# Kernel tuning notes

Measured on AMD Instinct MI355X. Metric: run time of the kernel, lower is better.

Reference implementation:

```python
import jax, jax.numpy as jnp
from jax import lax
import numpy as np

# GConv2d config (matches init_kwargs)
OUT_TRANSFORMS = 4  # rotations: 0, 90, 180, 270 degrees
STRIDE = 1
PADDING = 1


def setup_inputs() -> dict:
    key = jax.random.key(0)
    k1, k2, k3, k4 = jax.random.split(key, 4)
    B, IC_EFF, H, W = 16, 256, 64, 64   # IC_EFF = in_channels * in_transformations
    OC, K, F = 64, 4, 3                 # out_channels, num_dynamic_kernels, filter_size
    x = jax.random.normal(k1, (B, IC_EFF, H, W), dtype=jnp.float32)
    W_fc = jax.random.normal(k2, (K, IC_EFF), dtype=jnp.float32) * (1.0 / np.sqrt(IC_EFF))
    b_fc = jnp.zeros((K,), dtype=jnp.float32)
    kernel_bank = jax.random.normal(k3, (K, OC, IC_EFF, F, F), dtype=jnp.float32)
    return {"x": x, "W_fc": W_fc, "b_fc": b_fc, "kernel_bank": kernel_bank}


def reference(x, W_fc, b_fc, kernel_bank):
    B, C, H, W = x.shape
    # Dynamic routing: global average pool -> linear -> softmax over kernel bank
    pooled = x.mean(axis=(2, 3))                      # [B, C]
    coeffs = jax.nn.softmax(pooled @ W_fc.T + b_fc, axis=1)  # [B, K]
    # Sample-specific base kernels: mix of kernel bank
    base = jnp.einsum('bk,kocij->bocij', coeffs, kernel_bank)  # [B, oc, C, f, f]
    # P4 orientation expansion: rotate kernel spatially, stack along out-channels
    oriented = jnp.concatenate(
        [jnp.rot90(base, k, axes=(-2, -1)) for k in range(OUT_TRANSFORMS)], axis=1
    )  # [B, 4*oc, C, f, f]
    O, f = oriented.shape[1], oriented.shape[-1]
    # Batched per-sample conv via grouped convolution (one launch instead of B)
    xg = x.reshape(1, B * C, H, W)
    kg = oriented.reshape(B * O, C, f, f)
    out = lax.conv_general_dilated(
        xg, kg,
        window_strides=(STRIDE, STRIDE),
        padding=[(PADDING, PADDING), (PADDING, PADDING)],
        dimension_numbers=('NCHW', 'OIHW', 'NCHW'),
        feature_group_count=B,
    )  # [1, B*O, H', W']
    Ho, Wo = out.shape[-2], out.shape[-1]
    return out.reshape(B, O, Ho, Wo)
```

## Files before the change

### kernel.cpp

```cpp
#include <hip/hip_runtime.h>

#define B_  16
#define C_  256
#define O_  256

typedef short    bf16x8 __attribute__((ext_vector_type(8)));
typedef float    f32x16 __attribute__((ext_vector_type(16)));
typedef unsigned u32x4  __attribute__((ext_vector_type(4)));
typedef unsigned u32x2  __attribute__((ext_vector_type(2)));

#define XROW_SH  1056
#define XBC_SH   (66 * XROW_SH)
#define XT_BYTES ((size_t)B_ * 16 * XBC_SH * 2)

#define WTILE_SH 9216
#define WORP_BYTES ((size_t)B_ * 16 * 4 * WTILE_SH * 2)

#define XBUF_SH  10752

__device__ __forceinline__ unsigned cvtpk(float lo, float hi) {
    unsigned r;
    asm("v_cvt_pk_bf16_f32 %0, %1, %2" : "=v"(r) : "v"(lo), "v"(hi));
    return r;
}

__device__ __forceinline__ void gload16(const void* g, void* l) {
    __builtin_amdgcn_global_load_lds(
        (const __attribute__((address_space(1))) unsigned int*)g,
        (__attribute__((address_space(3))) unsigned int*)l, 16, 0, 0);
}

__global__ __launch_bounds__(256) void xprep_kernel(const float* __restrict__ x,
                                                    short* __restrict__ xT,
                                                    float* __restrict__ pooled4) {
    const int cg = blockIdx.x;
    const int b  = blockIdx.y;
    const int z  = blockIdx.z;
    const int t  = threadIdx.x;
    const int lane = t & 63, wv = t >> 6;
    const int cc = cg >> 1, lh = cg & 1;

    short* xTb = xT + (size_t)(b * 16 + cc) * XBC_SH;
    const float* xb = x + ((size_t)(b * C_ + cg * 8) << 12);

    {
        u32x4 zv = {0, 0, 0, 0};
        if (t < 32) {
            int r   = z * 16 + 1 + (t >> 1);
            int col = (t & 1) ? 65 : 0;
            *(u32x4*)&xTb[r * XROW_SH + lh * 528 + col * 8] = zv;
        }
        if (z == 0 || z == 3) {
            int row = (z == 0) ? 0 : 65;
            if (t < 66) *(u32x4*)&xTb[row * XROW_SH + lh * 528 + t * 8] = zv;
        }
    }

    float s[8] = {0.f, 0.f, 0.f, 0.f, 0.f, 0.f, 0.f, 0.f};
    const int px = lane;
#pragma unroll
    for (int r = 0; r < 4; ++r) {
        const int row = z * 16 + wv * 4 + r;
        const float* src = xb + row * 64 + px;
        float v[8];
#pragma unroll
        for (int i = 0; i < 8; ++i) { v[i] = src[(size_t)i << 12]; s[i] += v[i]; }
        u32x4 d = { cvtpk(v[0], v[1]), cvtpk(v[2], v[3]),
                    cvtpk(v[4], v[5]), cvtpk(v[6], v[7]) };
        *(u32x4*)&xTb[(row + 1) * XROW_SH + lh * 528 + (px + 1) * 8] = d;
    }

#pragma unroll
    for (int i = 0; i < 8; ++i)
#pragma unroll
        for (int off = 32; off; off >>= 1) s[i] += __shfl_xor(s[i], off, 64);

    __shared__ float pr[4][8];
    if (lane == 0) {
#pragma unroll
        for (int i = 0; i < 8; ++i) pr[wv][i] = s[i];
    }
    __syncthreads();
    if (t < 8) {
        float v = pr[0][t] + pr[1][t] + pr[2][t] + pr[3][t];
        pooled4[(z * B_ + b) * C_ + cg * 8 + t] = v * (1.0f / 4096.0f);
    }
}

__global__ __launch_bounds__(256) void mix_kernel(const float* __restrict__ bank,
                                                  const float* __restrict__ pooled4,
                                                  const float* __restrict__ W_fc,
                                                  const float* __restrict__ b_fc,
                                                  short* __restrict__ worp) {
    const int b  = blockIdx.x;
    const int cc = blockIdx.y;
    const int t  = threadIdx.x, lane = t & 63, wid = t >> 6;

    __shared__ float bankL[4 * 64 * 37];
    __shared__ float lg[4];

    {
        float s = 0.f;
#pragma unroll
        for (int q = 0; q < 4; ++q) {
            int c = lane * 4 + q;
            float pv = pooled4[b * C_ + c] + pooled4[(B_ + b) * C_ + c]
                     + pooled4[(2 * B_ + b) * C_ + c] + pooled4[(3 * B_ + b) * C_ + c];
            s += pv * W_fc[wid * C_ + c];
        }
#pragma unroll
        for (int off = 32; off; off >>= 1) s += __shfl_down(s, off, 64);
        if (lane == 0) lg[wid] = s + b_fc[wid];
    }
    __syncthreads();
    float l0 = lg[0], l1 = lg[1], l2 = lg[2], l3 = lg[3];
    float mx = fmaxf(fmaxf(l0, l1), fmaxf(l2, l3));
    float e0 = expf(l0 - mx), e1 = expf(l1 - mx), e2 = expf(l2 - mx), e3 = expf(l3 - mx);
    float inv = 1.f / (e0 + e1 + e2 + e3);
    const float cf0 = e0 * inv, cf1 = e1 * inv, cf2 = e2 * inv, cf3 = e3 * inv;

    const int oq  = t >> 6;
    const int o64 = t & 63;

    for (int sub = 0; sub < 4; ++sub) {
        __syncthreads();
        for (int i = t; i < 9216; i += 256) {
            int run = i / 36, e = i % 36;
            bankL[run * 37 + e] = bank[((size_t)run * C_ + cc * 16 + sub * 4) * 9 + e];
        }
        __syncthreads();

        const int lhs = sub >> 1;
        const float* bp = &bankL[o64 * 37];
#pragma unroll
        for (int ti = 0; ti < 3; ++ti)
#pragma unroll
            for (int tj = 0; tj < 3; ++tj) {
                int si, sj;
                if      (oq == 0) { si = ti;     sj = tj;     }
                else if (oq == 1) { si = tj;     sj = 2 - ti; }
                else if (oq == 2) { si = 2 - ti; sj = 2 - tj; }
                else              { si = 2 - tj; sj = ti;     }
                const int sij = si * 3 + sj;
                float v[4];
#pragma unroll
                for (int c4 = 0; c4 < 4; ++c4) {
                    const float* q = bp + c4 * 9 + sij;
                    v[c4] = cf0 * q[0] + cf1 * q[64 * 37] + cf2 * q[2 * 64 * 37]
                          + cf3 * q[3 * 64 * 37];
                }
                u32x2 d = { cvtpk(v[0], v[1]), cvtpk(v[2], v[3]) };
                size_t base = (((((size_t)(b * 16 + cc) * 4 + oq) * 9 + (ti * 3 + tj)) * 2
                                + lhs) * 64 + o64) * 8 + (sub & 1) * 4;
                *(u32x2*)&worp[base] = d;
            }
    }
}

__global__ __launch_bounds__(256, 2)
void conv_mfma(const short* __restrict__ xT, const short* __restrict__ worp,
               float* __restrict__ out) {
    __shared__ short lds[2 * XBUF_SH];

    const int g    = blockIdx.x;
    const int w    = (g & 7) * 64 + (g >> 3);
    const int oq   = w & 3;
    const int m    = w >> 2;
    const int rowt = m & 7;
    const int b    = m >> 3;
    const int y0   = rowt * 8;

    const int t    = threadIdx.x;
    const int lane = t & 63;
    const int wid  = t >> 6;
    const int l31  = lane & 31;
    const int lh   = lane >> 5;

    const char* xsrcB = (const char*)xT
        + ((size_t)(b * 16) * XBC_SH + (size_t)y0 * XROW_SH) * 2 + lane * 16;
    const short* wq = worp + (((size_t)(b * 16) * 4) + oq) * WTILE_SH;

#define STAGE(ccc, p)                                                           \
    { const char* xs = xsrcB + (size_t)(ccc) * (XBC_SH * 2);                    \
      char* xd = (char*)lds + (p) * (XBUF_SH * 2);                              \
      for (int u = wid; u < 21; u += 4) gload16(xs + u * 1024, xd + u * 1024); }

#define BRD(r, s) (*(const bf16x8*)&xcur[(((r) * 2 + lh) * 66 + (s) + l31) * 8])

    f32x16 acc0[4] = {}, acc1[4] = {};

    STAGE(0, 0);
    __syncthreads();

    for (int cc = 0; cc < 16; ++cc) {
        const int p = cc & 1;
        const short* wsc = wq + (size_t)cc * (4 * WTILE_SH);

        bf16x8 Af[3][3][2];
#pragma unroll
        for (int i = 0; i < 3; ++i)
#pragma unroll
            for (int j = 0; j < 3; ++j)
#pragma unroll
                for (int oh = 0; oh < 2; ++oh)
                    Af[i][j][oh] = *(const bf16x8*)
                        (wsc + (((i * 3 + j) * 2 + lh) * 64 + oh * 32 + l31) * 8);

        if (cc < 15) STAGE(cc + 1, p ^ 1);

        const short* xcur = lds + p * XBUF_SH;
        __builtin_amdgcn_s_setprio(1);
#pragma unroll
        for (int i = 0; i < 3; ++i)
#pragma unroll
            for (int j = 0; j < 3; ++j) {
                bf16x8 B00 = BRD(2 * wid + i,     j);
                bf16x8 B01 = BRD(2 * wid + i,     32 + j);
                bf16x8 B10 = BRD(2 * wid + i + 1, j);
                bf16x8 B11 = BRD(2 * wid + i + 1, 32 + j);
                acc0[0] = __builtin_amdgcn_mfma_f32_32x32x16_bf16(Af[i][j][0], B00, acc0[0], 0, 0, 0);
                acc1[0] = __builtin_amdgcn_mfma_f32_32x32x16_bf16(Af[i][j][1], B00, acc1[0], 0, 0, 0);
                acc0[1] = __builtin_amdgcn_mfma_f32_32x32x16_bf16(Af[i][j][0], B01, acc0[1], 0, 0, 0);
                acc1[1] = __builtin_amdgcn_mfma_f32_32x32x16_bf16(Af[i][j][1], B01, acc1[1], 0, 0, 0);
                acc0[2] = __builtin_amdgcn_mfma_f32_32x32x16_bf16(Af[i][j][0], B10, acc0[2], 0, 0, 0);
                acc1[2] = __builtin_amdgcn_mfma_f32_32x32x16_bf16(Af[i][j][1], B10, acc1[2], 0, 0, 0);
                acc0[3] = __builtin_amdgcn_mfma_f32_32x32x16_bf16(Af[i][j][0], B11, acc0[3], 0, 0, 0);
                acc1[3] = __builtin_amdgcn_mfma_f32_32x32x16_bf16(Af[i][j][1], B11, acc1[3], 0, 0, 0);
            }
        __builtin_amdgcn_s_setprio(0);
        __syncthreads();
    }
#undef STAGE
#undef BRD

#pragma unroll
    for (int pf = 0; pf < 4; ++pf) {
        const int yb  = y0 + 2 * wid + (pf >> 1);
        const int xcb = 32 * (pf & 1) + l31;
#pragma unroll
        for (int r = 0; r < 16; ++r) {
            const int orow = (r & 3) + 8 * (r >> 2) + 4 * lh;
            const int o0   = oq * 64 + orow;
            __builtin_nontemporal_store(acc0[pf][r],
                &out[((size_t)(b * O_ + o0)      << 12) + yb * 64 + xcb]);
            __builtin_nontemporal_store(acc1[pf][r],
                &out[((size_t)(b * O_ + o0 + 32) << 12) + yb * 64 + xcb]);
        }
    }
}

extern "C" void kernel_launch(void* const* d_in, const int* in_sizes, int n_in,
                              void* d_out, int out_size, void* d_ws, size_t ws_size,
                              hipStream_t stream) {
    const float* x    = (const float*)d_in[0];
    const float* W_fc = (const float*)d_in[1];
    const float* b_fc = (const float*)d_in[2];
    const float* bank = (const float*)d_in[3];
    float* out = (float*)d_out;

    short* xTb     = (short*)d_ws;
    short* worp    = (short*)((char*)d_ws + XT_BYTES);
    float* pooled4 = (float*)((char*)d_ws + XT_BYTES + WORP_BYTES);

    xprep_kernel<<<dim3(32, 16, 4), 256, 0, stream>>>(x, xTb, pooled4);
    mix_kernel<<<dim3(B_, 16), 256, 0, stream>>>(bank, pooled4, W_fc, b_fc, worp);
    conv_mfma<<<512, 256, 0, stream>>>(xTb, worp, out);
}
```

Before: 115.7 us.

## Stage weight tiles through LDS and split MFMA loop into barriered row phases

Weight tiles for each channel chunk are now asynchronously copied into a second double-buffered LDS region alongside the input tile, instead of being read straight from global memory into registers. The compute loop is reorganized into three phases, one per filter row. Each phase reuses the input rows already held in registers and loads only one new row, with barriers and sched_barrier between phases to interleave LDS reads with MFMAs. This aims to hide global weight load latency and cut register pressure. It costs about 36 KB more LDS per block, which could limit occupancy at two blocks per CU, and adds extra block-wide barriers.

After: 111.5 us. -3.6%, faster.

```diff
diff --git a/kernel.cpp b/kernel.cpp
--- a/kernel.cpp
+++ b/kernel.cpp
@@ -160,7 +160,7 @@
 __global__ __launch_bounds__(256, 2)
 void conv_mfma(const short* __restrict__ xT, const short* __restrict__ worp,
                float* __restrict__ out) {
-    __shared__ short lds[2 * XBUF_SH];
+    __shared__ short lds[2 * XBUF_SH + 2 * WTILE_SH];
 
     const int g    = blockIdx.x;
     const int w    = (g & 7) * 64 + (g >> 3);
@@ -178,14 +178,42 @@
 
     const char* xsrcB = (const char*)xT
         + ((size_t)(b * 16) * XBC_SH + (size_t)y0 * XROW_SH) * 2 + lane * 16;
-    const short* wq = worp + (((size_t)(b * 16) * 4) + oq) * WTILE_SH;
+    const char* wsrcB = (const char*)worp
+        + (((size_t)(b * 16) * 4) + oq) * (WTILE_SH * 2) + lane * 16;
 
 #define STAGE(ccc, p)                                                           \
     { const char* xs = xsrcB + (size_t)(ccc) * (XBC_SH * 2);                    \
+      const char* ws = wsrcB + (size_t)(ccc) * (4 * WTILE_SH * 2);              \
       char* xd = (char*)lds + (p) * (XBUF_SH * 2);                              \
-      for (int u = wid; u < 21; u += 4) gload16(xs + u * 1024, xd + u * 1024); }
+      char* wd = (char*)lds + 2 * (XBUF_SH * 2) + (p) * (WTILE_SH * 2);         \
+      for (int u = wid; u < 21; u += 4) gload16(xs + u * 1024, xd + u * 1024);  \
+      for (int u = wid; u < 18; u += 4) gload16(ws + u * 1024, wd + u * 1024); }
 
 #define BRD(r, s) (*(const bf16x8*)&xcur[(((r) * 2 + lh) * 66 + (s) + l31) * 8])
+#define LOADROW(R, r)                                                           \
+    { R[0] = BRD(r, 0);  R[1] = BRD(r, 1);  R[2] = BRD(r, 2);                   \
+      R[3] = BRD(r, 32); R[4] = BRD(r, 33); R[5] = BRD(r, 34); }
+
+#define TAPROW(i, RA, RB)                                                       \
+    _Pragma("unroll")                                                           \
+    for (int j = 0; j < 3; ++j) {                                               \
+        const int tap = (i) * 3 + j;                                            \
+        const short* wp = wcur + ((tap * 2 + lh) * 64 + l31) * 8;               \
+        bf16x8 A0 = *(const bf16x8*)wp;                                         \
+        bf16x8 A1 = *(const bf16x8*)(wp + 256);                                 \
+        acc0[0] = __builtin_amdgcn_mfma_f32_32x32x16_bf16(A0, RA[j],     acc0[0], 0, 0, 0); \
+        acc1[0] = __builtin_amdgcn_mfma_f32_32x32x16_bf16(A1, RA[j],     acc1[0], 0, 0, 0); \
+        acc0[1] = __builtin_amdgcn_mfma_f32_32x32x16_bf16(A0, RA[3 + j], acc0[1], 0, 0, 0); \
+        acc1[1] = __builtin_amdgcn_mfma_f32_32x32x16_bf16(A1, RA[3 + j], acc1[1], 0, 0, 0); \
+        acc0[2] = __builtin_amdgcn_mfma_f32_32x32x16_bf16(A0, RB[j],     acc0[2], 0, 0, 0); \
+        acc1[2] = __builtin_amdgcn_mfma_f32_32x32x16_bf16(A1, RB[j],     acc1[2], 0, 0, 0); \
+        acc0[3] = __builtin_amdgcn_mfma_f32_32x32x16_bf16(A0, RB[3 + j], acc0[3], 0, 0, 0); \
+        acc1[3] = __builtin_amdgcn_mfma_f32_32x32x16_bf16(A1, RB[3 + j], acc1[3], 0, 0, 0); \
+    }
+
+#define PHASE_EDGE()                                                            \
+    __builtin_amdgcn_sched_barrier(0);                                          \
+    __builtin_amdgcn_s_barrier();
 
     f32x16 acc0[4] = {}, acc1[4] = {};
 
@@ -194,44 +222,34 @@
 
     for (int cc = 0; cc < 16; ++cc) {
         const int p = cc & 1;
-        const short* wsc = wq + (size_t)cc * (4 * WTILE_SH);
-
-        bf16x8 Af[3][3][2];
-#pragma unroll
-        for (int i = 0; i < 3; ++i)
-#pragma unroll
-            for (int j = 0; j < 3; ++j)
-#pragma unroll
-                for (int oh = 0; oh < 2; ++oh)
-                    Af[i][j][oh] = *(const bf16x8*)
-                        (wsc + (((i * 3 + j) * 2 + lh) * 64 + oh * 32 + l31) * 8);
-
+        const short* xcur = lds + p * XBUF_SH;
+        const short* wcur = lds + 2 * XBUF_SH + p * WTILE_SH;
+
+        bf16x8 R0[6], R1[6];
+        LOADROW(R0, 2 * wid);
+        LOADROW(R1, 2 * wid + 1);
         if (cc < 15) STAGE(cc + 1, p ^ 1);
-
-        const short* xcur = lds + p * XBUF_SH;
+        PHASE_EDGE();
         __builtin_amdgcn_s_setprio(1);
-#pragma unroll
-        for (int i = 0; i < 3; ++i)
-#pragma unroll
-            for (int j = 0; j < 3; ++j) {
-                bf16x8 B00 = BRD(2 * wid + i,     j);
-                bf16x8 B01 = BRD(2 * wid + i,     32 + j);
-                bf16x8 B10 = BRD(2 * wid + i + 1, j);
-                bf16x8 B11 = BRD(2 * wid + i + 1, 32 + j);
-                acc0[0] = __builtin_amdgcn_mfma_f32_32x32x16_bf16(Af[i][j][0], B00, acc0[0], 0, 0, 0);
-                acc1[0] = __builtin_amdgcn_mfma_f32_32x32x16_bf16(Af[i][j][1], B00, acc1[0], 0, 0, 0);
-                acc0[1] = __builtin_amdgcn_mfma_f32_32x32x16_bf16(Af[i][j][0], B01, acc0[1], 0, 0, 0);
-                acc1[1] = __builtin_amdgcn_mfma_f32_32x32x16_bf16(Af[i][j][1], B01, acc1[1], 0, 0, 0);
-                acc0[2] = __builtin_amdgcn_mfma_f32_32x32x16_bf16(Af[i][j][0], B10, acc0[2], 0, 0, 0);
-                acc1[2] = __builtin_amdgcn_mfma_f32_32x32x16_bf16(Af[i][j][1], B10, acc1[2], 0, 0, 0);
-                acc0[3] = __builtin_amdgcn_mfma_f32_32x32x16_bf16(Af[i][j][0], B11, acc0[3], 0, 0, 0);
-                acc1[3] = __builtin_amdgcn_mfma_f32_32x32x16_bf16(Af[i][j][1], B11, acc1[3], 0, 0, 0);
-            }
+        TAPROW(0, R0, R1)
+        __builtin_amdgcn_s_setprio(0);
+        LOADROW(R0, 2 * wid + 2);
+        PHASE_EDGE();
+        __builtin_amdgcn_s_setprio(1);
+        TAPROW(1, R1, R0)
+        __builtin_amdgcn_s_setprio(0);
+        LOADROW(R1, 2 * wid + 3);
+        PHASE_EDGE();
+        __builtin_amdgcn_s_setprio(1);
+        TAPROW(2, R0, R1)
         __builtin_amdgcn_s_setprio(0);
         __syncthreads();
     }
 #undef STAGE
 #undef BRD
+#undef LOADROW
+#undef TAPROW
+#undef PHASE_EDGE
 
 #pragma unroll
     for (int pf = 0; pf < 4; ++pf) {
```
